# Optimization experiments

Hardware: AMD Instinct MI355X
Metric: run time of the kernel (lower is better)

Reference implementation:

```python
import jax, jax.numpy as jnp
import numpy as np

B_SZ, SEQ, D_IN, D_ST, D_OUT = 16, 8192, 128, 128, 128


def setup_inputs() -> dict:
    key = jax.random.key(0)
    ku, ka, kb, kc, kd = jax.random.split(key, 5)
    u = jax.random.normal(ku, (B_SZ, SEQ, D_IN), dtype=jnp.float32)
    # A scaled to spectral radius ~0.9 so the long recurrence stays stable
    A = jax.random.normal(ka, (D_ST, D_ST), dtype=jnp.float32) * (0.9 / np.sqrt(D_ST))
    B = jax.random.normal(kb, (D_ST, D_IN), dtype=jnp.float32) * (1.0 / np.sqrt(D_IN))
    C = jax.random.normal(kc, (D_OUT, D_ST), dtype=jnp.float32) * (1.0 / np.sqrt(D_ST))
    D = jax.random.normal(kd, (D_OUT, D_IN), dtype=jnp.float32) * (1.0 / np.sqrt(D_IN))
    return {"u": u, "A": A, "B": B, "C": C, "D": D}


def reference(u, A, B, C, D):
    # x_t = x_{t-1} A^T + u_t B^T ; y_t = x_t C^T + u_t D^T ; x_0 = 0
    batch = u.shape[0]
    state0 = jnp.zeros((batch, A.shape[0]), dtype=u.dtype)

    def step(state, u_t):  # state: [B, S_dim], u_t: [B, D_in]
        new_state = state @ A.T + u_t @ B.T
        y = new_state @ C.T + u_t @ D.T
        return new_state, y

    u_t_first = jnp.swapaxes(u, 0, 1)  # [SEQ, B, D_in]
    _, ys = jax.lax.scan(step, state0, u_t_first)
    return jnp.swapaxes(ys, 0, 1)  # [B, SEQ, D_out]
```

## Files before the change

kernel.cpp:

```cpp
#include <hip/hip_runtime.h>


#define SEQ 8192
#define BS  16
#define DD  128
#define CL  32
#define NC  256
#define GRP 16
#define NG  16

typedef __bf16 bf16t;
typedef __bf16 bf16x8 __attribute__((ext_vector_type(8)));
typedef __bf16 bf16x4 __attribute__((ext_vector_type(4)));
typedef float  f32x4  __attribute__((ext_vector_type(4)));

#define MFMA(a,b,c) __builtin_amdgcn_mfma_f32_16x16x32_bf16(a,b,c,0,0,0)

__device__ __forceinline__ int swz(int b, int j) { return j ^ ((b & 7) << 3); }

struct Frag { bf16x8 h[4]; bf16x8 l[4]; };

__device__ __forceinline__ void load_frag_T(const float* __restrict__ src, int lane, int w, Frag& f) {
    int n  = (w << 4) + (lane & 15);
    int kb = ((lane >> 4) & 3) << 3;
#pragma unroll
    for (int q = 0; q < 4; q++) {
        const float* p = src + n * DD + (q << 5) + kb;
#pragma unroll
        for (int e = 0; e < 8; e++) {
            float v = p[e];
            bf16t hh = (bf16t)v;
            f.h[q][e] = hh;
            f.l[q][e] = (bf16t)(v - (float)hh);
        }
    }
}

__device__ __forceinline__ void load_frag_N(const float* __restrict__ src, int lane, int w, Frag& f) {
    int n  = (w << 4) + (lane & 15);
    int kb = ((lane >> 4) & 3) << 3;
#pragma unroll
    for (int q = 0; q < 4; q++) {
#pragma unroll
        for (int e = 0; e < 8; e++) {
            float v = src[((q << 5) + kb + e) * DD + n];
            bf16t hh = (bf16t)v;
            f.h[q][e] = hh;
            f.l[q][e] = (bf16t)(v - (float)hh);
        }
    }
}

__device__ __forceinline__ bf16x8 afrag(const bf16t* __restrict__ X, int lane, int q) {
    int b  = lane & 15;
    int j0 = (q << 5) + (((lane >> 4) & 3) << 3);
    return *(const bf16x8*)(X + b * DD + swz(b, j0));
}

__device__ __forceinline__ void put_state(bf16t* __restrict__ H, bf16t* __restrict__ L,
                                          int lane, int w, f32x4 acc) {
    int n = (w << 4) + (lane & 15);
#pragma unroll
    for (int r = 0; r < 4; r++) {
        int b = (((lane >> 4) & 3) << 2) + r;
        float v = acc[r];
        bf16t hh = (bf16t)v;
        H[b * DD + swz(b, n)] = hh;
        L[b * DD + swz(b, n)] = (bf16t)(v - (float)hh);
    }
}

__device__ __forceinline__ void stage_rows(const float* __restrict__ src, long rs,
                                           bf16t* __restrict__ H, bf16t* __restrict__ L, int tid) {
    int b  = tid >> 5;
    int j0 = (tid & 31) << 2;
    float4 v = *(const float4*)(src + (long)b * rs + j0);
    float vv[4] = { v.x, v.y, v.z, v.w };
    bf16x4 h, l;
#pragma unroll
    for (int e = 0; e < 4; e++) {
        bf16t hh = (bf16t)vv[e];
        h[e] = hh;
        l[e] = (bf16t)(vv[e] - (float)hh);
    }
    *(bf16x4*)(H + b * DD + swz(b, j0)) = h;
    *(bf16x4*)(L + b * DD + swz(b, j0)) = l;
}

__device__ __forceinline__ f32x4 load_accfrag(const float* __restrict__ src, int lane, int w) {
    int n = (w << 4) + (lane & 15);
    f32x4 a;
#pragma unroll
    for (int r = 0; r < 4; r++) {
        int b = (((lane >> 4) & 3) << 2) + r;
        a[r] = src[b * DD + n];
    }
    return a;
}

__device__ __forceinline__ void store_accfrag(float* __restrict__ dst, int lane, int w,
                                              f32x4 a, long rs) {
    int n = (w << 4) + (lane & 15);
#pragma unroll
    for (int r = 0; r < 4; r++) {
        int b = (((lane >> 4) & 3) << 2) + r;
        dst[(long)b * rs + n] = a[r];
    }
}

__global__ __launch_bounds__(512) void k_chunk(const float* __restrict__ u,
                                               const float* __restrict__ A,
                                               const float* __restrict__ B,
                                               float* __restrict__ E,
                                               float* __restrict__ P) {
    __shared__ __align__(16) bf16t Xh[2][BS * DD], Xl[2][BS * DD];
    __shared__ __align__(16) bf16t Uh[2][BS * DD], Ul[2][BS * DD];
    int tid = threadIdx.x, lane = tid & 63, w = tid >> 6;
    bool ident = blockIdx.x >= NC;
    int g2 = blockIdx.x - NC;

    Frag fA, fB;
    load_frag_T(A, lane, w, fA);
    if (!ident) load_frag_T(B, lane, w, fB);

    for (int i = tid; i < BS * DD; i += 512) {
        int b = i >> 7, j = swz(b, i & 127);
        float v = (ident && j == g2 * 16 + b) ? 1.f : 0.f;
        Xh[0][i] = (bf16t)v;
        Xl[0][i] = (bf16t)0.f;
    }
    int c = blockIdx.x;
    const float* ubase = u + (long)c * CL * DD;
    int b_ = tid >> 5, j0_ = (tid & 31) << 2;
    if (!ident) stage_rows(ubase, (long)SEQ * DD, Uh[0], Ul[0], tid);
    __syncthreads();

    int p = 0;
    f32x4 acc = {0.f, 0.f, 0.f, 0.f};
    for (int i = 0; i < CL; i++) {
        float4 un = {0.f, 0.f, 0.f, 0.f};
        if (!ident && i + 1 < CL)
            un = *(const float4*)(ubase + (long)b_ * SEQ * DD + (i + 1) * DD + j0_);
        f32x4 ax = {0.f,0.f,0.f,0.f}, ax2 = {0.f,0.f,0.f,0.f};
#pragma unroll
        for (int q = 0; q < 4; q++) {
            bf16x8 xh = afrag(Xh[p], lane, q), xl = afrag(Xl[p], lane, q);
            ax  = MFMA(xh, fA.h[q], ax);
            ax2 = MFMA(xl, fA.h[q], ax2);
            ax  = MFMA(xh, fA.l[q], ax);
            if (!ident) {
                bf16x8 uh = afrag(Uh[i & 1], lane, q), ul = afrag(Ul[i & 1], lane, q);
                ax2 = MFMA(uh, fB.h[q], ax2);
                ax  = MFMA(ul, fB.h[q], ax);
                ax2 = MFMA(uh, fB.l[q], ax2);
            }
        }
        acc = ax + ax2;
        if (i + 1 < CL) {
            put_state(Xh[p ^ 1], Xl[p ^ 1], lane, w, acc);
            if (!ident) {
                float vv[4] = { un.x, un.y, un.z, un.w };
                bf16x4 h, l;
#pragma unroll
                for (int e = 0; e < 4; e++) {
                    bf16t hh = (bf16t)vv[e];
                    h[e] = hh;
                    l[e] = (bf16t)(vv[e] - (float)hh);
                }
                *(bf16x4*)(Uh[(i + 1) & 1] + b_ * DD + swz(b_, j0_)) = h;
                *(bf16x4*)(Ul[(i + 1) & 1] + b_ * DD + swz(b_, j0_)) = l;
            }
            __syncthreads();
            p ^= 1;
        }
    }
    if (!ident) store_accfrag(E + (long)c * BS * DD, lane, w, acc, DD);
    else        store_accfrag(P + (long)g2 * 16 * DD, lane, w, acc, DD);
}

__global__ __launch_bounds__(512) void k_group(const float* __restrict__ E,
                                               const float* __restrict__ P,
                                               float* __restrict__ E2,
                                               float* __restrict__ Pg) {
    __shared__ __align__(16) bf16t Xh[2][BS * DD], Xl[2][BS * DD];
    int tid = threadIdx.x, lane = tid & 63, w = tid >> 6;
    bool ident = blockIdx.x >= NG;
    int g2 = blockIdx.x - NG;
    Frag fP;
    load_frag_N(P, lane, w, fP);
    for (int i = tid; i < BS * DD; i += 512) {
        int b = i >> 7, j = swz(b, i & 127);
        float v = (ident && j == g2 * 16 + b) ? 1.f : 0.f;
        Xh[0][i] = (bf16t)v;
        Xl[0][i] = (bf16t)0.f;
    }
    __syncthreads();
    int p = 0, g = blockIdx.x;
    f32x4 acc = {0.f, 0.f, 0.f, 0.f};
    for (int r = 0; r < GRP; r++) {
        f32x4 a1 = {0.f,0.f,0.f,0.f}, a2 = {0.f,0.f,0.f,0.f};
        if (!ident) a1 = load_accfrag(E + (long)(g * GRP + r) * BS * DD, lane, w);
#pragma unroll
        for (int q = 0; q < 4; q++) {
            bf16x8 xh = afrag(Xh[p], lane, q), xl = afrag(Xl[p], lane, q);
            a1 = MFMA(xh, fP.h[q], a1);
            a2 = MFMA(xl, fP.h[q], a2);
            a1 = MFMA(xh, fP.l[q], a1);
        }
        acc = a1 + a2;
        if (r + 1 < GRP) {
            put_state(Xh[p ^ 1], Xl[p ^ 1], lane, w, acc);
            __syncthreads();
            p ^= 1;
        }
    }
    if (!ident) store_accfrag(E2 + (long)g * BS * DD, lane, w, acc, DD);
    else        store_accfrag(Pg + (long)g2 * 16 * DD, lane, w, acc, DD);
}

__global__ __launch_bounds__(512) void k_top(const float* __restrict__ E2,
                                             const float* __restrict__ Pg,
                                             float* __restrict__ S2) {
    __shared__ __align__(16) bf16t Xh[2][BS * DD], Xl[2][BS * DD];
    int tid = threadIdx.x, lane = tid & 63, w = tid >> 6;
    Frag fP;
    load_frag_N(Pg, lane, w, fP);
    for (int i = tid; i < BS * DD; i += 512) {
        Xh[0][i] = (bf16t)0.f;
        Xl[0][i] = (bf16t)0.f;
    }
    __syncthreads();
    int p = 0;
    f32x4 T = {0.f, 0.f, 0.f, 0.f};
    for (int g = 0; g < NG; g++) {
        store_accfrag(S2 + (long)g * BS * DD, lane, w, T, DD);
        f32x4 a1 = load_accfrag(E2 + (long)g * BS * DD, lane, w), a2 = {0.f,0.f,0.f,0.f};
#pragma unroll
        for (int q = 0; q < 4; q++) {
            bf16x8 xh = afrag(Xh[p], lane, q), xl = afrag(Xl[p], lane, q);
            a1 = MFMA(xh, fP.h[q], a1);
            a2 = MFMA(xl, fP.h[q], a2);
            a1 = MFMA(xh, fP.l[q], a1);
        }
        T = a1 + a2;
        if (g + 1 < NG) {
            put_state(Xh[p ^ 1], Xl[p ^ 1], lane, w, T);
            __syncthreads();
            p ^= 1;
        }
    }
}

__global__ __launch_bounds__(512) void k_fix(const float* __restrict__ E,
                                             const float* __restrict__ P,
                                             const float* __restrict__ S2,
                                             float* __restrict__ S) {
    __shared__ __align__(16) bf16t Xh[2][BS * DD], Xl[2][BS * DD];
    int tid = threadIdx.x, lane = tid & 63, w = tid >> 6;
    int g = blockIdx.x;
    Frag fP;
    load_frag_N(P, lane, w, fP);
    stage_rows(S2 + (long)g * BS * DD, DD, Xh[0], Xl[0], tid);
    f32x4 T = load_accfrag(S2 + (long)g * BS * DD, lane, w);
    __syncthreads();
    int p = 0;
    for (int r = 0; r < GRP; r++) {
        int c = g * GRP + r;
        store_accfrag(S + (long)c * BS * DD, lane, w, T, DD);
        if (r + 1 == GRP) break;
        f32x4 a1 = load_accfrag(E + (long)c * BS * DD, lane, w), a2 = {0.f,0.f,0.f,0.f};
#pragma unroll
        for (int q = 0; q < 4; q++) {
            bf16x8 xh = afrag(Xh[p], lane, q), xl = afrag(Xl[p], lane, q);
            a1 = MFMA(xh, fP.h[q], a1);
            a2 = MFMA(xl, fP.h[q], a2);
            a1 = MFMA(xh, fP.l[q], a1);
        }
        T = a1 + a2;
        put_state(Xh[p ^ 1], Xl[p ^ 1], lane, w, T);
        __syncthreads();
        p ^= 1;
    }
}

__global__ __launch_bounds__(512) void k_main(const float* __restrict__ u,
                                              const float* __restrict__ A,
                                              const float* __restrict__ B,
                                              const float* __restrict__ C,
                                              const float* __restrict__ D,
                                              const float* __restrict__ S,
                                              float* __restrict__ out) {
    __shared__ __align__(16) bf16t Xh[2][BS * DD], Xl[2][BS * DD];
    __shared__ __align__(16) bf16t Uh[2][BS * DD], Ul[2][BS * DD];
    int tid = threadIdx.x, lane = tid & 63, w = tid >> 6;
    Frag fA, fB, fC, fD;
    load_frag_T(A, lane, w, fA);
    load_frag_T(B, lane, w, fB);
    load_frag_T(C, lane, w, fC);
    load_frag_T(D, lane, w, fD);
    int c = blockIdx.x;
    const float* ubase = u + (long)c * CL * DD;
    int b_ = tid >> 5, j0_ = (tid & 31) << 2;
    stage_rows(S + (long)c * BS * DD, DD, Xh[0], Xl[0], tid);
    stage_rows(ubase, (long)SEQ * DD, Uh[0], Ul[0], tid);
    __syncthreads();
    int p = 0;
    for (int i = 0; i < CL; i++) {
        float4 un = {0.f, 0.f, 0.f, 0.f};
        if (i + 1 < CL)
            un = *(const float4*)(ubase + (long)b_ * SEQ * DD + (i + 1) * DD + j0_);
        f32x4 ax = {0.f,0.f,0.f,0.f}, ax2 = {0.f,0.f,0.f,0.f};
        f32x4 ay = {0.f,0.f,0.f,0.f}, ay2 = {0.f,0.f,0.f,0.f};
#pragma unroll
        for (int q = 0; q < 4; q++) {
            bf16x8 xh = afrag(Xh[p], lane, q), xl = afrag(Xl[p], lane, q);
            bf16x8 uh = afrag(Uh[i & 1], lane, q), ul = afrag(Ul[i & 1], lane, q);
            ax  = MFMA(xh, fA.h[q], ax);
            ax2 = MFMA(xl, fA.h[q], ax2);
            ax  = MFMA(xh, fA.l[q], ax);
            ax2 = MFMA(uh, fB.h[q], ax2);
            ax  = MFMA(ul, fB.h[q], ax);
            ax2 = MFMA(uh, fB.l[q], ax2);
            ay  = MFMA(uh, fD.h[q], ay);
            ay2 = MFMA(ul, fD.h[q], ay2);
            ay  = MFMA(uh, fD.l[q], ay);
        }
        f32x4 xnew = ax + ax2;
        put_state(Xh[p ^ 1], Xl[p ^ 1], lane, w, xnew);
        if (i + 1 < CL) {
            float vv[4] = { un.x, un.y, un.z, un.w };
            bf16x4 h, l;
#pragma unroll
            for (int e = 0; e < 4; e++) {
                bf16t hh = (bf16t)vv[e];
                h[e] = hh;
                l[e] = (bf16t)(vv[e] - (float)hh);
            }
            *(bf16x4*)(Uh[(i + 1) & 1] + b_ * DD + swz(b_, j0_)) = h;
            *(bf16x4*)(Ul[(i + 1) & 1] + b_ * DD + swz(b_, j0_)) = l;
        }
        __syncthreads();
#pragma unroll
        for (int q = 0; q < 4; q++) {
            bf16x8 nh = afrag(Xh[p ^ 1], lane, q), nl = afrag(Xl[p ^ 1], lane, q);
            ay  = MFMA(nh, fC.h[q], ay);
            ay2 = MFMA(nl, fC.h[q], ay2);
            ay  = MFMA(nh, fC.l[q], ay);
        }
        f32x4 y = ay + ay2;
        store_accfrag(out + ((long)c * CL + i) * DD, lane, w, y, (long)SEQ * DD);
        p ^= 1;
    }
}

extern "C" void kernel_launch(void* const* d_in, const int* in_sizes, int n_in,
                              void* d_out, int out_size, void* d_ws, size_t ws_size,
                              hipStream_t stream) {
    (void)in_sizes; (void)n_in; (void)out_size; (void)ws_size;
    const float* u = (const float*)d_in[0];
    const float* A = (const float*)d_in[1];
    const float* B = (const float*)d_in[2];
    const float* C = (const float*)d_in[3];
    const float* D = (const float*)d_in[4];
    float* out = (float*)d_out;
    float* ws  = (float*)d_ws;
    float* P  = ws;
    float* Pg = ws + 16384;
    float* E  = ws + 32768;
    float* E2 = ws + 32768 + 524288;
    float* S2 = E2 + 32768;
    float* S  = S2 + 32768;
    dim3 blk(512);
    k_chunk<<<NC + 8, blk, 0, stream>>>(u, A, B, E, P);
    k_group<<<NG + 8, blk, 0, stream>>>(E, P, E2, Pg);
    k_top  <<<1,      blk, 0, stream>>>(E2, Pg, S2);
    k_fix  <<<NG,     blk, 0, stream>>>(E, P, S2, S);
    k_main <<<NC,     blk, 0, stream>>>(u, A, B, C, D, S, out);
}
```

Before: 131.7 us.

## Fold C into precomputed CA and CB+D, halve chunk length, drop low-order B/u splits

New measurement: 137.1 us. +4.1%, slower.

```diff
diff --git a/kernel.cpp b/kernel.cpp
--- a/kernel.cpp
+++ b/kernel.cpp
@@ -4,10 +4,10 @@
 #define SEQ 8192
 #define BS  16
 #define DD  128
-#define CL  32
-#define NC  256
+#define CL  16
+#define NC  512
 #define GRP 16
-#define NG  16
+#define NG  32
 
 typedef __bf16 bf16t;
 typedef __bf16 bf16x8 __attribute__((ext_vector_type(8)));
@@ -18,7 +18,8 @@
 
 __device__ __forceinline__ int swz(int b, int j) { return j ^ ((b & 7) << 3); }
 
-struct Frag { bf16x8 h[4]; bf16x8 l[4]; };
+struct Frag  { bf16x8 h[4]; bf16x8 l[4]; };
+struct FragH { bf16x8 h[4]; };
 
 __device__ __forceinline__ void load_frag_T(const float* __restrict__ src, int lane, int w, Frag& f) {
     int n  = (w << 4) + (lane & 15);
@@ -33,6 +34,17 @@
             f.h[q][e] = hh;
             f.l[q][e] = (bf16t)(v - (float)hh);
         }
+    }
+}
+
+__device__ __forceinline__ void load_frag_T_h(const float* __restrict__ src, int lane, int w, FragH& f) {
+    int n  = (w << 4) + (lane & 15);
+    int kb = ((lane >> 4) & 3) << 3;
+#pragma unroll
+    for (int q = 0; q < 4; q++) {
+        const float* p = src + n * DD + (q << 5) + kb;
+#pragma unroll
+        for (int e = 0; e < 8; e++) f.h[q][e] = (bf16t)p[e];
     }
 }
 
@@ -87,6 +99,14 @@
     *(bf16x4*)(L + b * DD + swz(b, j0)) = l;
 }
 
+__device__ __forceinline__ void write_u_h(bf16t* __restrict__ H, int b_, int j0_, float4 v) {
+    float vv[4] = { v.x, v.y, v.z, v.w };
+    bf16x4 h;
+#pragma unroll
+    for (int e = 0; e < 4; e++) h[e] = (bf16t)vv[e];
+    *(bf16x4*)(H + b_ * DD + swz(b_, j0_)) = h;
+}
+
 __device__ __forceinline__ f32x4 load_accfrag(const float* __restrict__ src, int lane, int w) {
     int n = (w << 4) + (lane & 15);
     f32x4 a;
@@ -108,68 +128,70 @@
     }
 }
 
-__global__ __launch_bounds__(512) void k_chunk(const float* __restrict__ u,
-                                               const float* __restrict__ A,
-                                               const float* __restrict__ B,
-                                               float* __restrict__ E,
-                                               float* __restrict__ P) {
-    __shared__ __align__(16) bf16t Xh[2][BS * DD], Xl[2][BS * DD];
-    __shared__ __align__(16) bf16t Uh[2][BS * DD], Ul[2][BS * DD];
-    int tid = threadIdx.x, lane = tid & 63, w = tid >> 6;
-    bool ident = blockIdx.x >= NC;
-    int g2 = blockIdx.x - NC;
-
-    Frag fA, fB;
+__global__ __launch_bounds__(128) void k_prepGH(const float* __restrict__ A,
+                                                const float* __restrict__ B,
+                                                const float* __restrict__ C,
+                                                const float* __restrict__ D,
+                                                float* __restrict__ Gm, float* __restrict__ Hm) {
+    int sel = blockIdx.x >> 7, r = blockIdx.x & 127, j = threadIdx.x;
+    const float* R = sel ? B : A;
+    float s = 0.f;
+#pragma unroll 8
+    for (int m = 0; m < 128; m++) s = fmaf(C[r * 128 + m], R[m * 128 + j], s);
+    if (sel) Hm[r * 128 + j] = s + D[r * 128 + j];
+    else     Gm[r * 128 + j] = s;
+}
+
+__global__ __launch_bounds__(512, 4) void k_chunk(const float* __restrict__ u,
+                                                  const float* __restrict__ A,
+                                                  const float* __restrict__ Bm,
+                                                  float* __restrict__ E,
+                                                  float* __restrict__ P) {
+    __shared__ __align__(16) bf16t Xh[2][BS * DD], Xl[2][BS * DD];
+    __shared__ __align__(16) bf16t Uh[2][BS * DD];
+    int tid = threadIdx.x, lane = tid & 63, w = tid >> 6;
+    bool ident = blockIdx.x < 8;
+    int g2 = blockIdx.x, c = blockIdx.x - 8;
+
+    Frag fA; FragH fB;
     load_frag_T(A, lane, w, fA);
-    if (!ident) load_frag_T(B, lane, w, fB);
+    if (!ident) load_frag_T_h(Bm, lane, w, fB);
 
     for (int i = tid; i < BS * DD; i += 512) {
         int b = i >> 7, j = swz(b, i & 127);
-        float v = (ident && j == g2 * 16 + b) ? 1.f : 0.f;
-        Xh[0][i] = (bf16t)v;
+        Xh[0][i] = (bf16t)((ident && j == g2 * 16 + b) ? 1.f : 0.f);
         Xl[0][i] = (bf16t)0.f;
     }
-    int c = blockIdx.x;
     const float* ubase = u + (long)c * CL * DD;
     int b_ = tid >> 5, j0_ = (tid & 31) << 2;
-    if (!ident) stage_rows(ubase, (long)SEQ * DD, Uh[0], Ul[0], tid);
+    if (!ident) {
+        float4 v0 = *(const float4*)(ubase + (long)b_ * SEQ * DD + j0_);
+        write_u_h(Uh[0], b_, j0_, v0);
+    }
     __syncthreads();
 
     int p = 0;
     f32x4 acc = {0.f, 0.f, 0.f, 0.f};
     for (int i = 0; i < CL; i++) {
-        float4 un = {0.f, 0.f, 0.f, 0.f};
+        float4 un = {0, 0, 0, 0};
         if (!ident && i + 1 < CL)
             un = *(const float4*)(ubase + (long)b_ * SEQ * DD + (i + 1) * DD + j0_);
-        f32x4 ax = {0.f,0.f,0.f,0.f}, ax2 = {0.f,0.f,0.f,0.f};
+        f32x4 ax = {0,0,0,0}, ax2 = {0,0,0,0};
 #pragma unroll
         for (int q = 0; q < 4; q++) {
             bf16x8 xh = afrag(Xh[p], lane, q), xl = afrag(Xl[p], lane, q);
             ax  = MFMA(xh, fA.h[q], ax);
             ax2 = MFMA(xl, fA.h[q], ax2);
-            ax  = MFMA(xh, fA.l[q], ax);
+            ax2 = MFMA(xh, fA.l[q], ax2);
             if (!ident) {
-                bf16x8 uh = afrag(Uh[i & 1], lane, q), ul = afrag(Ul[i & 1], lane, q);
-                ax2 = MFMA(uh, fB.h[q], ax2);
-                ax  = MFMA(ul, fB.h[q], ax);
-                ax2 = MFMA(uh, fB.l[q], ax2);
+                bf16x8 uh = afrag(Uh[i & 1], lane, q);
+                ax = MFMA(uh, fB.h[q], ax);
             }
         }
         acc = ax + ax2;
         if (i + 1 < CL) {
             put_state(Xh[p ^ 1], Xl[p ^ 1], lane, w, acc);
-            if (!ident) {
-                float vv[4] = { un.x, un.y, un.z, un.w };
-                bf16x4 h, l;
-#pragma unroll
-                for (int e = 0; e < 4; e++) {
-                    bf16t hh = (bf16t)vv[e];
-                    h[e] = hh;
-                    l[e] = (bf16t)(vv[e] - (float)hh);
-                }
-                *(bf16x4*)(Uh[(i + 1) & 1] + b_ * DD + swz(b_, j0_)) = h;
-                *(bf16x4*)(Ul[(i + 1) & 1] + b_ * DD + swz(b_, j0_)) = l;
-            }
+            if (!ident) write_u_h(Uh[(i + 1) & 1], b_, j0_, un);
             __syncthreads();
             p ^= 1;
         }
@@ -190,8 +212,7 @@
     load_frag_N(P, lane, w, fP);
     for (int i = tid; i < BS * DD; i += 512) {
         int b = i >> 7, j = swz(b, i & 127);
-        float v = (ident && j == g2 * 16 + b) ? 1.f : 0.f;
-        Xh[0][i] = (bf16t)v;
+        Xh[0][i] = (bf16t)((ident && j == g2 * 16 + b) ? 1.f : 0.f);
         Xl[0][i] = (bf16t)0.f;
     }
     __syncthreads();
@@ -232,9 +253,12 @@
     __syncthreads();
     int p = 0;
     f32x4 T = {0.f, 0.f, 0.f, 0.f};
+    f32x4 e2 = load_accfrag(E2, lane, w);
     for (int g = 0; g < NG; g++) {
         store_accfrag(S2 + (long)g * BS * DD, lane, w, T, DD);
-        f32x4 a1 = load_accfrag(E2 + (long)g * BS * DD, lane, w), a2 = {0.f,0.f,0.f,0.f};
+        if (g + 1 == NG) break;
+        f32x4 e2n = load_accfrag(E2 + (long)(g + 1) * BS * DD, lane, w);
+        f32x4 a1 = e2, a2 = {0.f,0.f,0.f,0.f};
 #pragma unroll
         for (int q = 0; q < 4; q++) {
             bf16x8 xh = afrag(Xh[p], lane, q), xl = afrag(Xl[p], lane, q);
@@ -243,18 +267,16 @@
             a1 = MFMA(xh, fP.l[q], a1);
         }
         T = a1 + a2;
-        if (g + 1 < NG) {
-            put_state(Xh[p ^ 1], Xl[p ^ 1], lane, w, T);
-            __syncthreads();
-            p ^= 1;
-        }
-    }
-}
-
-__global__ __launch_bounds__(512) void k_fix(const float* __restrict__ E,
+        put_state(Xh[p ^ 1], Xl[p ^ 1], lane, w, T);
+        __syncthreads();
+        p ^= 1;
+        e2 = e2n;
+    }
+}
+
+__global__ __launch_bounds__(512) void k_fix(float* __restrict__ E,
                                              const float* __restrict__ P,
-                                             const float* __restrict__ S2,
-                                             float* __restrict__ S) {
+                                             const float* __restrict__ S2) {
     __shared__ __align__(16) bf16t Xh[2][BS * DD], Xl[2][BS * DD];
     int tid = threadIdx.x, lane = tid & 63, w = tid >> 6;
     int g = blockIdx.x;
@@ -265,10 +287,11 @@
     __syncthreads();
     int p = 0;
     for (int r = 0; r < GRP; r++) {
-        int c = g * GRP + r;
-        store_accfrag(S + (long)c * BS * DD, lane, w, T, DD);
-        if (r + 1 == GRP) break;
-        f32x4 a1 = load_accfrag(E + (long)c * BS * DD, lane, w), a2 = {0.f,0.f,0.f,0.f};
+        long c = (long)(g * GRP + r) * BS * DD;
+        if (r + 1 == GRP) { store_accfrag(E + c, lane, w, T, DD); break; }
+        f32x4 a1 = load_accfrag(E + c, lane, w);
+        store_accfrag(E + c, lane, w, T, DD);
+        f32x4 a2 = {0.f,0.f,0.f,0.f};
 #pragma unroll
         for (int q = 0; q < 4; q++) {
             bf16x8 xh = afrag(Xh[p], lane, q), xl = afrag(Xl[p], lane, q);
@@ -283,73 +306,60 @@
     }
 }
 
-__global__ __launch_bounds__(512) void k_main(const float* __restrict__ u,
-                                              const float* __restrict__ A,
-                                              const float* __restrict__ B,
-                                              const float* __restrict__ C,
-                                              const float* __restrict__ D,
-                                              const float* __restrict__ S,
-                                              float* __restrict__ out) {
-    __shared__ __align__(16) bf16t Xh[2][BS * DD], Xl[2][BS * DD];
-    __shared__ __align__(16) bf16t Uh[2][BS * DD], Ul[2][BS * DD];
-    int tid = threadIdx.x, lane = tid & 63, w = tid >> 6;
-    Frag fA, fB, fC, fD;
+__global__ __launch_bounds__(512, 4) void k_main(const float* __restrict__ u,
+                                                 const float* __restrict__ A,
+                                                 const float* __restrict__ Bm,
+                                                 const float* __restrict__ Gm,
+                                                 const float* __restrict__ Hm,
+                                                 const float* __restrict__ S,
+                                                 float* __restrict__ out) {
+    __shared__ __align__(16) bf16t Xh[2][BS * DD], Xl[2][BS * DD];
+    __shared__ __align__(16) bf16t Uh[2][BS * DD];
+    int tid = threadIdx.x, lane = tid & 63, w = tid >> 6;
+    Frag fA; FragH fB, fG, fH;
     load_frag_T(A, lane, w, fA);
-    load_frag_T(B, lane, w, fB);
-    load_frag_T(C, lane, w, fC);
-    load_frag_T(D, lane, w, fD);
+    load_frag_T_h(Bm, lane, w, fB);
+    load_frag_T_h(Gm, lane, w, fG);
+    load_frag_T_h(Hm, lane, w, fH);
     int c = blockIdx.x;
     const float* ubase = u + (long)c * CL * DD;
     int b_ = tid >> 5, j0_ = (tid & 31) << 2;
     stage_rows(S + (long)c * BS * DD, DD, Xh[0], Xl[0], tid);
-    stage_rows(ubase, (long)SEQ * DD, Uh[0], Ul[0], tid);
+    {
+        float4 v0 = *(const float4*)(ubase + (long)b_ * SEQ * DD + j0_);
+        write_u_h(Uh[0], b_, j0_, v0);
+    }
     __syncthreads();
     int p = 0;
     for (int i = 0; i < CL; i++) {
-        float4 un = {0.f, 0.f, 0.f, 0.f};
+        float4 un = {0, 0, 0, 0};
         if (i + 1 < CL)
             un = *(const float4*)(ubase + (long)b_ * SEQ * DD + (i + 1) * DD + j0_);
-        f32x4 ax = {0.f,0.f,0.f,0.f}, ax2 = {0.f,0.f,0.f,0.f};
-        f32x4 ay = {0.f,0.f,0.f,0.f}, ay2 = {0.f,0.f,0.f,0.f};
-#pragma unroll
-        for (int q = 0; q < 4; q++) {
-            bf16x8 xh = afrag(Xh[p], lane, q), xl = afrag(Xl[p], lane, q);
-            bf16x8 uh = afrag(Uh[i & 1], lane, q), ul = afrag(Ul[i & 1], lane, q);
+        f32x4 ax = {0,0,0,0}, ax2 = {0,0,0,0};
+        f32x4 ay = {0,0,0,0}, ay2 = {0,0,0,0};
+#pragma unroll
+        for (int q = 0; q < 4; q++) {
+            bf16x8 xh = afrag(Xh[p], lane, q), xl = afrag(Xl[p], lane, q);
+            bf16x8 uh = afrag(Uh[i & 1], lane, q);
             ax  = MFMA(xh, fA.h[q], ax);
+            ax  = MFMA(uh, fB.h[q], ax);
             ax2 = MFMA(xl, fA.h[q], ax2);
-            ax  = MFMA(xh, fA.l[q], ax);
-            ax2 = MFMA(uh, fB.h[q], ax2);
-            ax  = MFMA(ul, fB.h[q], ax);
-            ax2 = MFMA(uh, fB.l[q], ax2);
-            ay  = MFMA(uh, fD.h[q], ay);
-            ay2 = MFMA(ul, fD.h[q], ay2);
-            ay  = MFMA(uh, fD.l[q], ay);
+            ax2 = MFMA(xh, fA.l[q], ax2);
+            ay  = MFMA(xh, fG.h[q], ay);
+            ay  = MFMA(uh, fH.h[q], ay);
+            ay2 = MFMA(xl, fG.h[q], ay2);
         }
         f32x4 xnew = ax + ax2;
-        put_state(Xh[p ^ 1], Xl[p ^ 1], lane, w, xnew);
         if (i + 1 < CL) {
-            float vv[4] = { un.x, un.y, un.z, un.w };
-            bf16x4 h, l;
-#pragma unroll
-            for (int e = 0; e < 4; e++) {
-                bf16t hh = (bf16t)vv[e];
-                h[e] = hh;
-                l[e] = (bf16t)(vv[e] - (float)hh);
-            }
-            *(bf16x4*)(Uh[(i + 1) & 1] + b_ * DD + swz(b_, j0_)) = h;
-            *(bf16x4*)(Ul[(i + 1) & 1] + b_ * DD + swz(b_, j0_)) = l;
-        }
-        __syncthreads();
-#pragma unroll
-        for (int q = 0; q < 4; q++) {
-            bf16x8 nh = afrag(Xh[p ^ 1], lane, q), nl = afrag(Xl[p ^ 1], lane, q);
-            ay  = MFMA(nh, fC.h[q], ay);
-            ay2 = MFMA(nl, fC.h[q], ay2);
-            ay  = MFMA(nh, fC.l[q], ay);
+            put_state(Xh[p ^ 1], Xl[p ^ 1], lane, w, xnew);
+            write_u_h(Uh[(i + 1) & 1], b_, j0_, un);
         }
         f32x4 y = ay + ay2;
         store_accfrag(out + ((long)c * CL + i) * DD, lane, w, y, (long)SEQ * DD);
-        p ^= 1;
+        if (i + 1 < CL) {
+            __syncthreads();
+            p ^= 1;
+        }
     }
 }
 
@@ -364,16 +374,18 @@
     const float* D = (const float*)d_in[4];
     float* out = (float*)d_out;
     float* ws  = (float*)d_ws;
-    float* P  = ws;
-    float* Pg = ws + 16384;
-    float* E  = ws + 32768;
-    float* E2 = ws + 32768 + 524288;
-    float* S2 = E2 + 32768;
-    float* S  = S2 + 32768;
+    float* Gm = ws;
+    float* Hm = Gm + 16384;
+    float* P  = Hm + 16384;
+    float* Pg = P  + 16384;
+    float* E  = Pg + 16384;
+    float* E2 = E  + 1048576;
+    float* S2 = E2 + 65536;
     dim3 blk(512);
+    k_prepGH<<<256, 128, 0, stream>>>(A, B, C, D, Gm, Hm);
     k_chunk<<<NC + 8, blk, 0, stream>>>(u, A, B, E, P);
     k_group<<<NG + 8, blk, 0, stream>>>(E, P, E2, Pg);
     k_top  <<<1,      blk, 0, stream>>>(E2, Pg, S2);
-    k_fix  <<<NG,     blk, 0, stream>>>(E, P, S2, S);
-    k_main <<<NC,     blk, 0, stream>>>(u, A, B, C, D, S, out);
-}
+    k_fix  <<<NG,     blk, 0, stream>>>(E, P, S2);
+    k_main <<<NC,     blk, 0, stream>>>(u, A, B, Gm, Hm, E, out);
+}
```
